# Kernel optimization log

Hardware: AMD Instinct MI355X
Metric: run time of the kernel (lower is better)

The kernel has to match this reference:

```python
import jax, jax.numpy as jnp
import numpy as np

N_NODES = 100000
N_EDGES = 1600000
D_IN = 128
D_HID = 128
D_OUT = 64


def spmm(vals, row, col, x):
    # sparse [N,N] @ dense [N,D]: out[r] = sum_e vals[e] * x[col[e]] for row[e]==r
    msgs = vals[:, None] * x[col]            # [E, D]
    return jax.ops.segment_sum(msgs, row, num_segments=N_NODES)


def setup_inputs() -> dict:
    key = jax.random.key(0)
    ks = jax.random.split(key, 8)
    x = jax.random.normal(ks[0], (N_NODES, D_IN), dtype=jnp.float32)
    vals = jax.random.uniform(ks[1], (N_EDGES,), dtype=jnp.float32)
    W1 = jax.random.normal(ks[2], (D_IN, D_HID), dtype=jnp.float32) * (1.0 / np.sqrt(D_IN))
    b1 = jnp.zeros((D_HID,), dtype=jnp.float32)
    W2 = jax.random.normal(ks[3], (D_HID, D_HID), dtype=jnp.float32) * (1.0 / np.sqrt(D_HID))
    b2 = jnp.zeros((D_HID,), dtype=jnp.float32)
    W3 = jax.random.normal(ks[4], (D_HID, D_OUT), dtype=jnp.float32) * (1.0 / np.sqrt(D_HID))
    b3 = jnp.zeros((D_OUT,), dtype=jnp.float32)
    row = jax.random.randint(ks[5], (N_EDGES,), 0, N_NODES, dtype=jnp.int32)
    col = jax.random.randint(ks[6], (N_EDGES,), 0, N_NODES, dtype=jnp.int32)
    return {"x": x, "vals": vals, "W1": W1, "b1": b1, "W2": W2, "b2": b2,
            "W3": W3, "b3": b3, "row": row, "col": col}


def reference(x, vals, W1, b1, W2, b2, W3, b3, row, col):
    # GCNConv 1: linear -> spmm -> relu
    h = jax.nn.relu(spmm(vals, row, col, x @ W1 + b1))
    # GCNConv 2: linear -> spmm -> relu
    h = jax.nn.relu(spmm(vals, row, col, h @ W2 + b2))
    # GCNConv 3 (output): linear -> spmm, no activation
    out = spmm(vals, row, col, h @ W3 + b3)
    return out
```

## Files before the change

kernel.cpp:

```cpp
#include <hip/hip_runtime.h>

#define N_NODES 100000
#define N_EDGES 1600000

#define NBK 782
#define EPB 8192
#define NBA 196
#define CAPE 4096

typedef __attribute__((ext_vector_type(8))) short short8;
typedef __attribute__((ext_vector_type(4))) float f32x4;

__device__ __forceinline__ ushort f2bf(float f) {
    uint u = __float_as_uint(f);
    return (ushort)((u + 0x7fff + ((u >> 16) & 1)) >> 16);
}
__device__ __forceinline__ float bflo(uint p) { return __uint_as_float(p << 16); }
__device__ __forceinline__ float bfhi(uint p) { return __uint_as_float(p & 0xffff0000u); }


__device__ void binA_body(int bid, const int* __restrict__ row,
                          const int* __restrict__ col, const float* __restrict__ vals,
                          int2* __restrict__ tmp, int* __restrict__ gcount,
                          int* __restrict__ offT) {
    __shared__ int h[NBK];
    __shared__ int cur[NBK];
    __shared__ int wpart[16];
    int t = threadIdx.x;
    int lane = t & 63;
    int base = bid * EPB;

    int rr[8], cc[8];
    float vv[8];
#pragma unroll
    for (int u = 0; u < 8; ++u) {
        int e = base + u * 1024 + t;
        bool ok = (e < N_EDGES);
        rr[u] = ok ? row[e] : -1;
        cc[u] = ok ? col[e] : 0;
        vv[u] = ok ? vals[e] : 0.f;
    }

    if (t < NBK) h[t] = 0;
    __syncthreads();
#pragma unroll
    for (int u = 0; u < 8; ++u)
        if (rr[u] >= 0) atomicAdd(&h[rr[u] >> 7], 1);
    __syncthreads();
    int hv = (t < NBK) ? h[t] : 0;
    if (hv) atomicAdd(&gcount[t], hv);

    int v = hv;
    for (int off = 1; off < 64; off <<= 1) {
        int u2 = __shfl_up(v, off);
        if (lane >= off) v += u2;
    }
    if (lane == 63) wpart[t >> 6] = v;
    __syncthreads();
    if (t == 0) {
        int acc = 0;
#pragma unroll
        for (int i = 0; i < 16; ++i) { int w = wpart[i]; wpart[i] = acc; acc += w; }
    }
    __syncthreads();
    v += wpart[t >> 6];
    if (t < NBK) {
        int ex = v - hv;
        cur[t] = ex;
        offT[t * NBA + bid] = ex;
    }
    if (t == NBK - 1) offT[NBK * NBA + bid] = v;
    __syncthreads();
#pragma unroll
    for (int u = 0; u < 8; ++u) {
        if (rr[u] >= 0) {
            int p = atomicAdd(&cur[rr[u] >> 7], 1);
            int2 w;
            w.x = ((rr[u] & 127) << 17) | cc[u];
            w.y = __float_as_int(vv[u]);
            tmp[base + p] = w;
        }
    }
}


__device__ void gemmA_body(int bid, const float* __restrict__ Xf,
                           const ushort* __restrict__ Wt,
                           const float* __restrict__ bias, ushort* __restrict__ Y) {
    int wv = threadIdx.x >> 6;
    int l = threadIdx.x & 63;
    int lg = l >> 4, lm = l & 15;
    int rbase = bid * 256 + wv * 16;

    int arow = rbase + lm;
    if (arow > N_NODES - 1) arow = N_NODES - 1;

    f32x4 acc[8];
#pragma unroll
    for (int n = 0; n < 8; n++) acc[n] = (f32x4){0.f, 0.f, 0.f, 0.f};

#pragma unroll
    for (int kk = 0; kk < 4; ++kk) {
        const float* ap = Xf + (size_t)arow * 128 + kk * 32 + lg * 8;
        float4 u = *(const float4*)ap;
        float4 v = *(const float4*)(ap + 4);
        short8 a = (short8){(short)f2bf(u.x), (short)f2bf(u.y), (short)f2bf(u.z),
                            (short)f2bf(u.w), (short)f2bf(v.x), (short)f2bf(v.y),
                            (short)f2bf(v.z), (short)f2bf(v.w)};
#pragma unroll
        for (int n = 0; n < 8; ++n) {
            short8 b = *(const short8*)(Wt + (size_t)(n * 16 + lm) * 128 + kk * 32 + lg * 8);
            acc[n] = __builtin_amdgcn_mfma_f32_16x16x32_bf16(a, b, acc[n], 0, 0, 0);
        }
    }

    int r0 = rbase + lg * 4;
#pragma unroll
    for (int n = 0; n < 8; ++n) {
        int c = n * 16 + lm;
        float bj = bias[c];
#pragma unroll
        for (int i = 0; i < 4; ++i) {
            int r = r0 + i;
            if (r < N_NODES) Y[(size_t)r * 128 + c] = f2bf(acc[n][i] + bj);
        }
    }
}

__global__ void __launch_bounds__(1024) fusedA_k(const int* __restrict__ row,
                                                 const int* __restrict__ col,
                                                 const float* __restrict__ vals,
                                                 int2* __restrict__ tmp,
                                                 int* __restrict__ gcount,
                                                 int* __restrict__ offT,
                                                 const float* __restrict__ x,
                                                 const ushort* __restrict__ Wt1,
                                                 const float* __restrict__ b1,
                                                 ushort* __restrict__ g) {
    if (blockIdx.x < NBA)
        binA_body(blockIdx.x, row, col, vals, tmp, gcount, offT);
    else
        gemmA_body(blockIdx.x - NBA, x, Wt1, b1, g);
}


__global__ void __launch_bounds__(256) binB_k(const int2* __restrict__ tmp,
                                              const int* __restrict__ offT,
                                              const int* __restrict__ gcount,
                                              int* __restrict__ rowptr,
                                              int2* __restrict__ ep) {
    __shared__ int goff[NBA];
    __shared__ int scnt[NBA];
    __shared__ int sdst[NBA];
    __shared__ int h[128];
    __shared__ int cur[128];
    __shared__ int2 ebuf[CAPE];
    __shared__ int wpart[4];
    __shared__ int wq[4];
    __shared__ int hp;
    int b = blockIdx.x, t = threadIdx.x;
    int lane = t & 63;

    int part = 0;
    for (int i = t; i < b; i += 256) part += gcount[i];
#pragma unroll
    for (int off = 1; off < 64; off <<= 1) part += __shfl_xor(part, off);
    if (lane == 0) wq[t >> 6] = part;
    if (b == 0 && t == 0) rowptr[N_NODES] = N_EDGES;

    int c = 0;
    if (t < NBA) {
        int o0 = offT[b * NBA + t];
        int o1 = offT[(b + 1) * NBA + t];
        c = o1 - o0;
        goff[t] = t * EPB + o0;
        scnt[t] = c;
    }
    int v = c;
    for (int off = 1; off < 64; off <<= 1) {
        int u = __shfl_up(v, off);
        if (lane >= off) v += u;
    }
    if (lane == 63) wpart[t >> 6] = v;
    if (t < 128) h[t] = 0;
    __syncthreads();
    if (t == 0) {
        int acc = 0;
#pragma unroll
        for (int i = 0; i < 4; ++i) { int w = wpart[i]; wpart[i] = acc; acc += w; }
    }
    __syncthreads();
    v += wpart[t >> 6];
    if (t < NBA) sdst[t] = v - c;
    __syncthreads();

    int grp = t >> 4, gl = t & 15;
    for (int s = grp; s < NBA; s += 16) {
        int n = scnt[s], go = goff[s], dd = sdst[s];
        for (int i = gl; i < n; i += 16) {
            int2 e = tmp[go + i];
            atomicAdd(&h[e.x >> 17], 1);
            ebuf[dd + i] = e;
        }
    }
    __syncthreads();
    int hv = (t < 128) ? h[t] : 0;
    int sv = hv;
    for (int off = 1; off < 64; off <<= 1) {
        int u = __shfl_up(sv, off);
        if (lane >= off) sv += u;
    }
    if (t == 63) hp = sv;
    __syncthreads();
    int bs = wq[0] + wq[1] + wq[2] + wq[3];
    if (t < 128) {
        int inc = sv + ((t >= 64) ? hp : 0);
        int ex = inc - hv;
        cur[t] = ex;
        int r = (b << 7) + t;
        if (r < N_NODES) rowptr[r] = bs + ex;
    }
    __syncthreads();
    int T = sdst[NBA - 1] + scnt[NBA - 1];
    for (int j = t; j < T; j += 256) {
        int2 e = ebuf[j];
        int p = atomicAdd(&cur[e.x >> 17], 1);
        int2 w;
        w.x = e.x & 0x1ffff;
        w.y = e.y;
        ep[bs + p] = w;
    }
}


__global__ void wcvt_k(const float* __restrict__ W1, const float* __restrict__ W2,
                       const float* __restrict__ W3, ushort* __restrict__ Wt1,
                       ushort* __restrict__ Wt2, ushort* __restrict__ Wt3,
                       int* __restrict__ gcount) {
    int i = blockIdx.x * 256 + threadIdx.x;
    if (i < NBK) gcount[i] = 0;
    if (i < 16384) {
        int n = i >> 7, k = i & 127;
        Wt1[i] = f2bf(W1[k * 128 + n]);
        Wt2[i] = f2bf(W2[k * 128 + n]);
    }
    if (i < 8192) {
        int n = i >> 7, k = i & 127;
        Wt3[i] = f2bf(W3[k * 64 + n]);
    }
}


template <int DN>
__global__ void __launch_bounds__(256) gemm_k(const ushort* __restrict__ Xb,
                                              const ushort* __restrict__ Wt,
                                              const float* __restrict__ bias,
                                              ushort* __restrict__ Y) {
    constexpr int NT = DN / 16;
    int wv = threadIdx.x >> 6;
    int l = threadIdx.x & 63;
    int lg = l >> 4, lm = l & 15;
    int rbase = blockIdx.x * 64 + wv * 16;

    int arow = rbase + lm;
    if (arow > N_NODES - 1) arow = N_NODES - 1;

    f32x4 acc[NT];
#pragma unroll
    for (int n = 0; n < NT; n++) acc[n] = (f32x4){0.f, 0.f, 0.f, 0.f};

#pragma unroll
    for (int kk = 0; kk < 4; ++kk) {
        short8 a = *(const short8*)(Xb + (size_t)arow * 128 + kk * 32 + lg * 8);
#pragma unroll
        for (int n = 0; n < NT; ++n) {
            short8 b = *(const short8*)(Wt + (size_t)(n * 16 + lm) * 128 + kk * 32 + lg * 8);
            acc[n] = __builtin_amdgcn_mfma_f32_16x16x32_bf16(a, b, acc[n], 0, 0, 0);
        }
    }

    int r0 = rbase + lg * 4;
#pragma unroll
    for (int n = 0; n < NT; ++n) {
        int c = n * 16 + lm;
        float bj = bias[c];
#pragma unroll
        for (int i = 0; i < 4; ++i) {
            int r = r0 + i;
            if (r < N_NODES) Y[(size_t)r * DN + c] = f2bf(acc[n][i] + bj);
        }
    }
}


#define SPMM_BODY(EPREAD)                                                     \
    if (D == 128) {                                                           \
        const uint4* xp = (const uint4*)xb;                                   \
        float a0 = 0.f, a1 = 0.f, a2 = 0.f, a3 = 0.f;                         \
        float a4 = 0.f, a5 = 0.f, a6 = 0.f, a7 = 0.f;                         \
        int i = s;                                                            \
        for (; i + 4 <= e; i += 4) {                                          \
            int2 e0 = EPREAD(i), e1 = EPREAD(i + 1);                          \
            int2 e2 = EPREAD(i + 2), e3 = EPREAD(i + 3);                      \
            uint4 x0 = xp[e0.x * 16 + hl];                                    \
            uint4 x1 = xp[e1.x * 16 + hl];                                    \
            uint4 x2 = xp[e2.x * 16 + hl];                                    \
            uint4 x3 = xp[e3.x * 16 + hl];                                    \
            float v0 = __int_as_float(e0.y), v1 = __int_as_float(e1.y);       \
            float v2 = __int_as_float(e2.y), v3 = __int_as_float(e3.y);       \
            a0 = fmaf(v0, bflo(x0.x), a0); a1 = fmaf(v0, bfhi(x0.x), a1);     \
            a2 = fmaf(v0, bflo(x0.y), a2); a3 = fmaf(v0, bfhi(x0.y), a3);     \
            a4 = fmaf(v0, bflo(x0.z), a4); a5 = fmaf(v0, bfhi(x0.z), a5);     \
            a6 = fmaf(v0, bflo(x0.w), a6); a7 = fmaf(v0, bfhi(x0.w), a7);     \
            a0 = fmaf(v1, bflo(x1.x), a0); a1 = fmaf(v1, bfhi(x1.x), a1);     \
            a2 = fmaf(v1, bflo(x1.y), a2); a3 = fmaf(v1, bfhi(x1.y), a3);     \
            a4 = fmaf(v1, bflo(x1.z), a4); a5 = fmaf(v1, bfhi(x1.z), a5);     \
            a6 = fmaf(v1, bflo(x1.w), a6); a7 = fmaf(v1, bfhi(x1.w), a7);     \
            a0 = fmaf(v2, bflo(x2.x), a0); a1 = fmaf(v2, bfhi(x2.x), a1);     \
            a2 = fmaf(v2, bflo(x2.y), a2); a3 = fmaf(v2, bfhi(x2.y), a3);     \
            a4 = fmaf(v2, bflo(x2.z), a4); a5 = fmaf(v2, bfhi(x2.z), a5);     \
            a6 = fmaf(v2, bflo(x2.w), a6); a7 = fmaf(v2, bfhi(x2.w), a7);     \
            a0 = fmaf(v3, bflo(x3.x), a0); a1 = fmaf(v3, bfhi(x3.x), a1);     \
            a2 = fmaf(v3, bflo(x3.y), a2); a3 = fmaf(v3, bfhi(x3.y), a3);     \
            a4 = fmaf(v3, bflo(x3.z), a4); a5 = fmaf(v3, bfhi(x3.z), a5);     \
            a6 = fmaf(v3, bflo(x3.w), a6); a7 = fmaf(v3, bfhi(x3.w), a7);     \
        }                                                                     \
        for (; i < e; ++i) {                                                  \
            int2 e0 = EPREAD(i);                                              \
            uint4 x0 = xp[e0.x * 16 + hl];                                    \
            float v0 = __int_as_float(e0.y);                                  \
            a0 = fmaf(v0, bflo(x0.x), a0); a1 = fmaf(v0, bfhi(x0.x), a1);     \
            a2 = fmaf(v0, bflo(x0.y), a2); a3 = fmaf(v0, bfhi(x0.y), a3);     \
            a4 = fmaf(v0, bflo(x0.z), a4); a5 = fmaf(v0, bfhi(x0.z), a5);     \
            a6 = fmaf(v0, bflo(x0.w), a6); a7 = fmaf(v0, bfhi(x0.w), a7);     \
        }                                                                     \
        if (RELU) {                                                           \
            a0 = fmaxf(a0, 0.f); a1 = fmaxf(a1, 0.f);                         \
            a2 = fmaxf(a2, 0.f); a3 = fmaxf(a3, 0.f);                         \
            a4 = fmaxf(a4, 0.f); a5 = fmaxf(a5, 0.f);                         \
            a6 = fmaxf(a6, 0.f); a7 = fmaxf(a7, 0.f);                         \
        }                                                                     \
        uint4 o;                                                              \
        o.x = (uint)f2bf(a0) | ((uint)f2bf(a1) << 16);                        \
        o.y = (uint)f2bf(a2) | ((uint)f2bf(a3) << 16);                        \
        o.z = (uint)f2bf(a4) | ((uint)f2bf(a5) << 16);                        \
        o.w = (uint)f2bf(a6) | ((uint)f2bf(a7) << 16);                        \
        ((uint4*)y)[w * 16 + hl] = o;                                         \
    } else {                                                                  \
        const uint2* xp = (const uint2*)xb;                                   \
        float a0 = 0.f, a1 = 0.f, a2 = 0.f, a3 = 0.f;                         \
        int i = s;                                                            \
        for (; i + 4 <= e; i += 4) {                                          \
            int2 e0 = EPREAD(i), e1 = EPREAD(i + 1);                          \
            int2 e2 = EPREAD(i + 2), e3 = EPREAD(i + 3);                      \
            uint2 x0 = xp[e0.x * 16 + hl];                                    \
            uint2 x1 = xp[e1.x * 16 + hl];                                    \
            uint2 x2 = xp[e2.x * 16 + hl];                                    \
            uint2 x3 = xp[e3.x * 16 + hl];                                    \
            float v0 = __int_as_float(e0.y), v1 = __int_as_float(e1.y);       \
            float v2 = __int_as_float(e2.y), v3 = __int_as_float(e3.y);       \
            a0 = fmaf(v0, bflo(x0.x), a0); a1 = fmaf(v0, bfhi(x0.x), a1);     \
            a2 = fmaf(v0, bflo(x0.y), a2); a3 = fmaf(v0, bfhi(x0.y), a3);     \
            a0 = fmaf(v1, bflo(x1.x), a0); a1 = fmaf(v1, bfhi(x1.x), a1);     \
            a2 = fmaf(v1, bflo(x1.y), a2); a3 = fmaf(v1, bfhi(x1.y), a3);     \
            a0 = fmaf(v2, bflo(x2.x), a0); a1 = fmaf(v2, bfhi(x2.x), a1);     \
            a2 = fmaf(v2, bflo(x2.y), a2); a3 = fmaf(v2, bfhi(x2.y), a3);     \
            a0 = fmaf(v3, bflo(x3.x), a0); a1 = fmaf(v3, bfhi(x3.x), a1);     \
            a2 = fmaf(v3, bflo(x3.y), a2); a3 = fmaf(v3, bfhi(x3.y), a3);     \
        }                                                                     \
        for (; i < e; ++i) {                                                  \
            int2 e0 = EPREAD(i);                                              \
            uint2 x0 = xp[e0.x * 16 + hl];                                    \
            float v0 = __int_as_float(e0.y);                                  \
            a0 = fmaf(v0, bflo(x0.x), a0); a1 = fmaf(v0, bfhi(x0.x), a1);     \
            a2 = fmaf(v0, bflo(x0.y), a2); a3 = fmaf(v0, bfhi(x0.y), a3);     \
        }                                                                     \
        if (RELU) {                                                           \
            a0 = fmaxf(a0, 0.f); a1 = fmaxf(a1, 0.f);                         \
            a2 = fmaxf(a2, 0.f); a3 = fmaxf(a3, 0.f);                         \
        }                                                                     \
        float4 o; o.x = a0; o.y = a1; o.z = a2; o.w = a3;                     \
        ((float4*)y)[w * 16 + hl] = o;                                        \
    }

template <int D, bool RELU>
__global__ void __launch_bounds__(256) spmm_k(const int* __restrict__ rowptr,
                                              const int2* __restrict__ ep,
                                              const ushort* __restrict__ xb,
                                              void* __restrict__ y) {
    constexpr int CAP = 1536;
    __shared__ int2 eb[CAP];
    __shared__ int sh_s0, sh_n;
    int t = threadIdx.x;
    int g = t >> 4, hl = t & 15;
    int rbase = blockIdx.x * 16;
    int w = rbase + g;

    if (t == 0) {
        int s0 = rowptr[rbase];
        int rend = rbase + 16; if (rend > N_NODES) rend = N_NODES;
        sh_s0 = s0;
        sh_n = rowptr[rend] - s0;
    }
    __syncthreads();
    int s0 = sh_s0, n = sh_n;
    bool inlds = (n <= CAP);
    if (inlds) {
        for (int j = t; j < n; j += 256) eb[j] = ep[s0 + j];
    }
    __syncthreads();
    if (w >= N_NODES) return;
    int s = rowptr[w], e = rowptr[w + 1];

    if (inlds) {
        s -= s0; e -= s0;
#define EPL(i) eb[i]
        SPMM_BODY(EPL)
#undef EPL
    } else {
#define EPG(i) ep[i]
        SPMM_BODY(EPG)
#undef EPG
    }
}


extern "C" void kernel_launch(void* const* d_in, const int* in_sizes, int n_in,
                              void* d_out, int out_size, void* d_ws, size_t ws_size,
                              hipStream_t stream) {
    const float* x    = (const float*)d_in[0];
    const float* vals = (const float*)d_in[1];
    const float* W1   = (const float*)d_in[2];
    const float* b1   = (const float*)d_in[3];
    const float* W2   = (const float*)d_in[4];
    const float* b2   = (const float*)d_in[5];
    const float* W3   = (const float*)d_in[6];
    const float* b3   = (const float*)d_in[7];
    const int* row    = (const int*)d_in[8];
    const int* col    = (const int*)d_in[9];
    float* out = (float*)d_out;

    char* ws = (char*)d_ws;
    int2*   ep     = (int2*)  (ws + 0);
    int*    rowptr = (int*)   (ws + 12800000);
    int*    gcount = (int*)   (ws + 13250000);
    ushort* Wt1    = (ushort*)(ws + 13601024);
    ushort* Wt2    = (ushort*)(ws + 13633792);
    ushort* Wt3    = (ushort*)(ws + 13666560);
    int*    offT   = (int*)   (ws + 13700096);
    ushort* g64    = (ushort*)(ws + 16000000);
    ushort* g      = (ushort*)(ws + 41600000);
    ushort* sbuf   = (ushort*)(ws + 67200000);

    int2* tmp = (int2*)sbuf;

    hipLaunchKernelGGL(wcvt_k, dim3(64), dim3(256), 0, stream,
                       W1, W2, W3, Wt1, Wt2, Wt3, gcount);

    const int GEMM1_BLKS = (N_NODES + 255) / 256;
    hipLaunchKernelGGL(fusedA_k, dim3(NBA + GEMM1_BLKS), dim3(1024), 0, stream,
                       row, col, vals, tmp, gcount, offT, x, Wt1, b1, g);

    hipLaunchKernelGGL(binB_k, dim3(NBK), dim3(256), 0, stream,
                       tmp, offT, gcount, rowptr, ep);

    const int GEMM_GRID = (N_NODES + 63) / 64;
    const int SPMM_GRID = (N_NODES + 15) / 16;

    hipLaunchKernelGGL((spmm_k<128, true>), dim3(SPMM_GRID), dim3(256), 0, stream,
                       rowptr, ep, g, sbuf);
    hipLaunchKernelGGL((gemm_k<128>), dim3(GEMM_GRID), dim3(256), 0, stream, sbuf, Wt2, b2, g);
    hipLaunchKernelGGL((spmm_k<128, true>), dim3(SPMM_GRID), dim3(256), 0, stream,
                       rowptr, ep, g, sbuf);
    hipLaunchKernelGGL((gemm_k<64>), dim3(GEMM_GRID), dim3(256), 0, stream, sbuf, Wt3, b3, g64);
    hipLaunchKernelGGL((spmm_k<64, false>), dim3(SPMM_GRID), dim3(256), 0, stream,
                       rowptr, ep, g64, out);
}
```

Baseline: 296.0 us.

## Move first GEMM into bin pass B and drop global bucket counter

The first dense GEMM moves from the bin pass A launch into the bin pass B launch, so pass A runs alone with only 196 blocks. The second pass reads its per-block prefix offsets from the offT table instead of a separately accumulated global counter. The global gcount array and its atomics are gone, and so is its zeroing in the weight-conversion kernel. Pass A now keeps the rank returned by the first shared atomic and reuses it, which removes a second round of shared atomics. The GEMM now uses 256-thread blocks covering 64 rows each, and pass A loses the overlap it had with the GEMM.

```diff
diff --git a/kernel.cpp b/kernel.cpp
--- a/kernel.cpp
+++ b/kernel.cpp
@@ -19,18 +19,19 @@
 __device__ __forceinline__ float bfhi(uint p) { return __uint_as_float(p & 0xffff0000u); }
 
 
-__device__ void binA_body(int bid, const int* __restrict__ row,
-                          const int* __restrict__ col, const float* __restrict__ vals,
-                          int2* __restrict__ tmp, int* __restrict__ gcount,
-                          int* __restrict__ offT) {
-    __shared__ int h[NBK];
-    __shared__ int cur[NBK];
+__global__ void __launch_bounds__(1024) binA_k(const int* __restrict__ row,
+                                               const int* __restrict__ col,
+                                               const float* __restrict__ vals,
+                                               int2* __restrict__ tmp,
+                                               int* __restrict__ offT) {
+    __shared__ int cnt[NBK];
+    __shared__ int exo[NBK];
     __shared__ int wpart[16];
     int t = threadIdx.x;
     int lane = t & 63;
-    int base = bid * EPB;
-
-    int rr[8], cc[8];
+    int base = blockIdx.x * EPB;
+
+    int rr[8], cc[8], rk[8];
     float vv[8];
 #pragma unroll
     for (int u = 0; u < 8; ++u) {
@@ -41,14 +42,13 @@
         vv[u] = ok ? vals[e] : 0.f;
     }
 
-    if (t < NBK) h[t] = 0;
+    if (t < NBK) cnt[t] = 0;
     __syncthreads();
 #pragma unroll
     for (int u = 0; u < 8; ++u)
-        if (rr[u] >= 0) atomicAdd(&h[rr[u] >> 7], 1);
-    __syncthreads();
-    int hv = (t < NBK) ? h[t] : 0;
-    if (hv) atomicAdd(&gcount[t], hv);
+        if (rr[u] >= 0) rk[u] = atomicAdd(&cnt[rr[u] >> 7], 1);
+    __syncthreads();
+    int hv = (t < NBK) ? cnt[t] : 0;
 
     int v = hv;
     for (int off = 1; off < 64; off <<= 1) {
@@ -66,15 +66,15 @@
     v += wpart[t >> 6];
     if (t < NBK) {
         int ex = v - hv;
-        cur[t] = ex;
-        offT[t * NBA + bid] = ex;
-    }
-    if (t == NBK - 1) offT[NBK * NBA + bid] = v;
+        exo[t] = ex;
+        offT[t * NBA + blockIdx.x] = ex;
+    }
+    if (t == NBK - 1) offT[NBK * NBA + blockIdx.x] = v;
     __syncthreads();
 #pragma unroll
     for (int u = 0; u < 8; ++u) {
         if (rr[u] >= 0) {
-            int p = atomicAdd(&cur[rr[u] >> 7], 1);
+            int p = exo[rr[u] >> 7] + rk[u];
             int2 w;
             w.x = ((rr[u] & 127) << 17) | cc[u];
             w.y = __float_as_int(vv[u]);
@@ -84,71 +84,9 @@
 }
 
 
-__device__ void gemmA_body(int bid, const float* __restrict__ Xf,
-                           const ushort* __restrict__ Wt,
-                           const float* __restrict__ bias, ushort* __restrict__ Y) {
-    int wv = threadIdx.x >> 6;
-    int l = threadIdx.x & 63;
-    int lg = l >> 4, lm = l & 15;
-    int rbase = bid * 256 + wv * 16;
-
-    int arow = rbase + lm;
-    if (arow > N_NODES - 1) arow = N_NODES - 1;
-
-    f32x4 acc[8];
-#pragma unroll
-    for (int n = 0; n < 8; n++) acc[n] = (f32x4){0.f, 0.f, 0.f, 0.f};
-
-#pragma unroll
-    for (int kk = 0; kk < 4; ++kk) {
-        const float* ap = Xf + (size_t)arow * 128 + kk * 32 + lg * 8;
-        float4 u = *(const float4*)ap;
-        float4 v = *(const float4*)(ap + 4);
-        short8 a = (short8){(short)f2bf(u.x), (short)f2bf(u.y), (short)f2bf(u.z),
-                            (short)f2bf(u.w), (short)f2bf(v.x), (short)f2bf(v.y),
-                            (short)f2bf(v.z), (short)f2bf(v.w)};
-#pragma unroll
-        for (int n = 0; n < 8; ++n) {
-            short8 b = *(const short8*)(Wt + (size_t)(n * 16 + lm) * 128 + kk * 32 + lg * 8);
-            acc[n] = __builtin_amdgcn_mfma_f32_16x16x32_bf16(a, b, acc[n], 0, 0, 0);
-        }
-    }
-
-    int r0 = rbase + lg * 4;
-#pragma unroll
-    for (int n = 0; n < 8; ++n) {
-        int c = n * 16 + lm;
-        float bj = bias[c];
-#pragma unroll
-        for (int i = 0; i < 4; ++i) {
-            int r = r0 + i;
-            if (r < N_NODES) Y[(size_t)r * 128 + c] = f2bf(acc[n][i] + bj);
-        }
-    }
-}
-
-__global__ void __launch_bounds__(1024) fusedA_k(const int* __restrict__ row,
-                                                 const int* __restrict__ col,
-                                                 const float* __restrict__ vals,
-                                                 int2* __restrict__ tmp,
-                                                 int* __restrict__ gcount,
-                                                 int* __restrict__ offT,
-                                                 const float* __restrict__ x,
-                                                 const ushort* __restrict__ Wt1,
-                                                 const float* __restrict__ b1,
-                                                 ushort* __restrict__ g) {
-    if (blockIdx.x < NBA)
-        binA_body(blockIdx.x, row, col, vals, tmp, gcount, offT);
-    else
-        gemmA_body(blockIdx.x - NBA, x, Wt1, b1, g);
-}
-
-
-__global__ void __launch_bounds__(256) binB_k(const int2* __restrict__ tmp,
-                                              const int* __restrict__ offT,
-                                              const int* __restrict__ gcount,
-                                              int* __restrict__ rowptr,
-                                              int2* __restrict__ ep) {
+__device__ void binB_body(int b, const int2* __restrict__ tmp,
+                          const int* __restrict__ offT, int* __restrict__ rowptr,
+                          int2* __restrict__ ep) {
     __shared__ int goff[NBA];
     __shared__ int scnt[NBA];
     __shared__ int sdst[NBA];
@@ -158,24 +96,23 @@
     __shared__ int wpart[4];
     __shared__ int wq[4];
     __shared__ int hp;
-    int b = blockIdx.x, t = threadIdx.x;
+    int t = threadIdx.x;
     int lane = t & 63;
 
-    int part = 0;
-    for (int i = t; i < b; i += 256) part += gcount[i];
-#pragma unroll
-    for (int off = 1; off < 64; off <<= 1) part += __shfl_xor(part, off);
-    if (lane == 0) wq[t >> 6] = part;
-    if (b == 0 && t == 0) rowptr[N_NODES] = N_EDGES;
-
-    int c = 0;
+    int o0 = 0, c = 0;
     if (t < NBA) {
-        int o0 = offT[b * NBA + t];
+        o0 = offT[b * NBA + t];
         int o1 = offT[(b + 1) * NBA + t];
         c = o1 - o0;
         goff[t] = t * EPB + o0;
         scnt[t] = c;
     }
+    int part = o0;
+#pragma unroll
+    for (int off = 1; off < 64; off <<= 1) part += __shfl_xor(part, off);
+    if (lane == 0) wq[t >> 6] = part;
+    if (b == 0 && t == 0) rowptr[N_NODES] = N_EDGES;
+
     int v = c;
     for (int off = 1; off < 64; off <<= 1) {
         int u = __shfl_up(v, off);
@@ -233,12 +170,68 @@
 }
 
 
+__device__ void gemm1_body(int bid, const float* __restrict__ Xf,
+                           const ushort* __restrict__ Wt,
+                           const float* __restrict__ bias, ushort* __restrict__ Y) {
+    int wv = threadIdx.x >> 6;
+    int l = threadIdx.x & 63;
+    int lg = l >> 4, lm = l & 15;
+    int rbase = bid * 64 + wv * 16;
+
+    int arow = rbase + lm;
+    if (arow > N_NODES - 1) arow = N_NODES - 1;
+
+    f32x4 acc[8];
+#pragma unroll
+    for (int n = 0; n < 8; n++) acc[n] = (f32x4){0.f, 0.f, 0.f, 0.f};
+
+#pragma unroll
+    for (int kk = 0; kk < 4; ++kk) {
+        const float* ap = Xf + (size_t)arow * 128 + kk * 32 + lg * 8;
+        float4 u = *(const float4*)ap;
+        float4 v = *(const float4*)(ap + 4);
+        short8 a = (short8){(short)f2bf(u.x), (short)f2bf(u.y), (short)f2bf(u.z),
+                            (short)f2bf(u.w), (short)f2bf(v.x), (short)f2bf(v.y),
+                            (short)f2bf(v.z), (short)f2bf(v.w)};
+#pragma unroll
+        for (int n = 0; n < 8; ++n) {
+            short8 b = *(const short8*)(Wt + (size_t)(n * 16 + lm) * 128 + kk * 32 + lg * 8);
+            acc[n] = __builtin_amdgcn_mfma_f32_16x16x32_bf16(a, b, acc[n], 0, 0, 0);
+        }
+    }
+
+    int r0 = rbase + lg * 4;
+#pragma unroll
+    for (int n = 0; n < 8; ++n) {
+        int c = n * 16 + lm;
+        float bj = bias[c];
+#pragma unroll
+        for (int i = 0; i < 4; ++i) {
+            int r = r0 + i;
+            if (r < N_NODES) Y[(size_t)r * 128 + c] = f2bf(acc[n][i] + bj);
+        }
+    }
+}
+
+__global__ void __launch_bounds__(256) fusedB_k(const int2* __restrict__ tmp,
+                                                const int* __restrict__ offT,
+                                                int* __restrict__ rowptr,
+                                                int2* __restrict__ ep,
+                                                const float* __restrict__ x,
+                                                const ushort* __restrict__ Wt1,
+                                                const float* __restrict__ b1,
+                                                ushort* __restrict__ g) {
+    if (blockIdx.x < NBK)
+        binB_body(blockIdx.x, tmp, offT, rowptr, ep);
+    else
+        gemm1_body(blockIdx.x - NBK, x, Wt1, b1, g);
+}
+
+
 __global__ void wcvt_k(const float* __restrict__ W1, const float* __restrict__ W2,
                        const float* __restrict__ W3, ushort* __restrict__ Wt1,
-                       ushort* __restrict__ Wt2, ushort* __restrict__ Wt3,
-                       int* __restrict__ gcount) {
+                       ushort* __restrict__ Wt2, ushort* __restrict__ Wt3) {
     int i = blockIdx.x * 256 + threadIdx.x;
-    if (i < NBK) gcount[i] = 0;
     if (i < 16384) {
         int n = i >> 7, k = i & 127;
         Wt1[i] = f2bf(W1[k * 128 + n]);
@@ -443,7 +436,6 @@
     char* ws = (char*)d_ws;
     int2*   ep     = (int2*)  (ws + 0);
     int*    rowptr = (int*)   (ws + 12800000);
-    int*    gcount = (int*)   (ws + 13250000);
     ushort* Wt1    = (ushort*)(ws + 13601024);
     ushort* Wt2    = (ushort*)(ws + 13633792);
     ushort* Wt3    = (ushort*)(ws + 13666560);
@@ -455,17 +447,16 @@
     int2* tmp = (int2*)sbuf;
 
     hipLaunchKernelGGL(wcvt_k, dim3(64), dim3(256), 0, stream,
-                       W1, W2, W3, Wt1, Wt2, Wt3, gcount);
-
-    const int GEMM1_BLKS = (N_NODES + 255) / 256;
-    hipLaunchKernelGGL(fusedA_k, dim3(NBA + GEMM1_BLKS), dim3(1024), 0, stream,
-                       row, col, vals, tmp, gcount, offT, x, Wt1, b1, g);
-
-    hipLaunchKernelGGL(binB_k, dim3(NBK), dim3(256), 0, stream,
-                       tmp, offT, gcount, rowptr, ep);
+                       W1, W2, W3, Wt1, Wt2, Wt3);
+
+    hipLaunchKernelGGL(binA_k, dim3(NBA), dim3(1024), 0, stream,
+                       row, col, vals, tmp, offT);
 
     const int GEMM_GRID = (N_NODES + 63) / 64;
     const int SPMM_GRID = (N_NODES + 15) / 16;
+
+    hipLaunchKernelGGL(fusedB_k, dim3(NBK + GEMM_GRID), dim3(256), 0, stream,
+                       tmp, offT, rowptr, ep, x, Wt1, b1, g);
 
     hipLaunchKernelGGL((spmm_k<128, true>), dim3(SPMM_GRID), dim3(256), 0, stream,
                        rowptr, ep, g, sbuf);
```

After: 290.0 us. 2.0% less time.
